# Performance work log

Hardware: AMD Instinct MI355X
Metric: run time of the kernel (lower is better)

## Reference

```python
import jax, jax.numpy as jnp
import numpy as np

B, N, D, H = 256, 1000, 128, 8
DH = D // H
TANH_CLIP = 10.0
NEG = -1e9  # finite stand-in for -inf mask fill (keeps grads clean)


def setup_inputs() -> dict:
    key = jax.random.key(0)
    ks = jax.random.split(key, 8)
    s = 1.0 / np.sqrt(D)
    return {
        "node_embeddings": jax.random.normal(ks[0], (B, N, D), jnp.float32),
        "W_node": jax.random.normal(ks[1], (D, 3 * D), jnp.float32) * s,   # project_node_embeddings
        "W_fixed": jax.random.normal(ks[2], (D, D), jnp.float32) * s,      # project_fixed_context
        "W_step": jax.random.normal(ks[3], (2 * D, D), jnp.float32) * s,   # project_step_context
        "W_out": jax.random.normal(ks[4], (D, D), jnp.float32) * s,        # project_out
        "prev_idx": jax.random.randint(ks[5], (B,), 0, N),
        "first_idx": jax.random.randint(ks[6], (B,), 0, N),
        "mask": jax.random.randint(ks[7], (B, N), 0, 2).astype(bool),      # True = masked/visited
    }


def reference(node_embeddings, W_node, W_fixed, W_step, W_out, prev_idx, first_idx, mask):
    b = jnp.arange(B)
    # Precompute fixed: context projection of graph embedding (mean aggregation)
    graph_embed = node_embeddings.mean(axis=1)                    # (B, D)
    fixed_context = graph_embed @ W_fixed                          # (B, D)
    # glimpse key / glimpse val / logit key from node embeddings
    kvl = node_embeddings @ W_node                                 # (B, N, 3D)
    glimpse_K, glimpse_V, logit_K = jnp.split(kvl, 3, axis=-1)
    gK = glimpse_K.reshape(B, N, H, DH)                            # (B, N, H, dh)
    gV = glimpse_V.reshape(B, N, H, DH)
    # Step context: cat(first node embed, last node embed) -> query
    step_ctx = jnp.concatenate(
        [node_embeddings[b, first_idx], node_embeddings[b, prev_idx]], axis=-1)  # (B, 2D)
    query = fixed_context + step_ctx @ W_step                      # (B, D)
    Q = query.reshape(B, H, DH)                                    # (B, H, dh)
    # Glimpse MHA (single query per batch element)
    compat = jnp.einsum("bhd,bnhd->bhn", Q, gK) / np.sqrt(DH)      # (B, H, N)
    compat = jnp.where(mask[:, None, :], NEG, compat)              # mask_inner
    attn = jax.nn.softmax(compat, axis=-1)
    heads = jnp.einsum("bhn,bnhd->bhd", attn, gV)                  # (B, H, dh)
    glimpse = heads.reshape(B, D) @ W_out                          # (B, D)
    # Logits against logit_K, tanh clipping, mask_logits, log-softmax
    logits = jnp.einsum("bd,bnd->bn", glimpse, logit_K) / np.sqrt(D)
    logits = TANH_CLIP * jnp.tanh(logits)
    logits = jnp.where(mask, NEG, logits)
    log_p = jax.nn.log_softmax(logits, axis=-1)                    # (B, N)
    return log_p
```

## Files before the change

kernel.cpp:

```cpp
#include <hip/hip_runtime.h>
#include <math.h>

#define BB 256
#define NN 1000
#define DD 128
#define HH 8
#define QQ 4
#define RQ 250
#define NEG -1e9f

#define SY_CNTA 0
#define SY_CNTC 1
#define SY_CNTE 2

__device__ __forceinline__ bool get_mask(const void* m, int flag, size_t idx) {
    if (flag == 1) return ((const int*)m)[idx] != 0;
    if (flag == 2) return ((const float*)m)[idx] != 0.0f;
    return ((const unsigned char*)m)[idx] != 0;
}

__device__ __forceinline__ void sy_barrier(int* p, int tid, int tgt) {
    if (tid == 0) {
        __builtin_amdgcn_fence(__ATOMIC_RELEASE, "agent");
        __hip_atomic_fetch_add(p, 1, __ATOMIC_RELAXED, __HIP_MEMORY_SCOPE_AGENT);
        while (__hip_atomic_load(p, __ATOMIC_RELAXED, __HIP_MEMORY_SCOPE_AGENT) < tgt)
            __builtin_amdgcn_s_sleep(8);
        __builtin_amdgcn_fence(__ATOMIC_ACQUIRE, "agent");
    }
    __syncthreads();
}

__global__ __launch_bounds__(256, 4) void k_one(
        const float* __restrict__ X, const float* __restrict__ Wnode,
        const float* __restrict__ Wfix, const float* __restrict__ Wstep,
        const float* __restrict__ Wout, const int* __restrict__ prev,
        const int* __restrict__ first, const void* __restrict__ mask,
        int* __restrict__ syg, float* __restrict__ partial,
        float* __restrict__ sqw, float* __restrict__ pvp,
        float* __restrict__ esumg, float* __restrict__ out) {
    const int bid = blockIdx.x, tid = threadIdx.x;
    const int b = bid >> 2, q = bid & 3;
    const int n0 = q * RQ;
    const size_t xoff = (size_t)b * NN * DD;
    int* sy = syg + b * 16;

    __shared__ __align__(16) float pool[4096];
    __shared__ __align__(16) float qks[HH][DD];
    __shared__ float gqv[DD];
    __shared__ float lgl[256];
    __shared__ unsigned short cidxL[256];
    __shared__ float redS[4][HH];
    __shared__ float Sh[HH];
    __shared__ float redw[4];
    __shared__ int wbase[4];
    __shared__ int s_flag, s_cnt;

    if (tid < 64) {
        const unsigned int* mw = (const unsigned int*)mask;
        unsigned int a0 = mw[tid], a1 = mw[tid + 64], a2 = mw[tid + 128], a3 = mw[tid + 192];
        int ii = (a0 <= 1u) && (a1 <= 1u) && (a2 <= 1u) && (a3 <= 1u);
        int ff = (a0 == 0u || a0 == 0x3F800000u) && (a1 == 0u || a1 == 0x3F800000u) &&
                 (a2 == 0u || a2 == 0x3F800000u) && (a3 == 0u || a3 == 0x3F800000u);
        int ai = __all(ii), af = __all(ff);
        if (tid == 0) s_flag = ai ? 1 : (af ? 2 : 0);
    }

    {
        float4* red4 = (float4*)pool;
        int c = tid & 31, s = tid >> 5;
        const float4* Xr = (const float4*)(X + xoff);
        float4 acc = make_float4(0.f, 0.f, 0.f, 0.f);
        for (int nl = s; nl < RQ; nl += 8) {
            float4 v = Xr[(n0 + nl) * 32 + c];
            acc.x += v.x; acc.y += v.y; acc.z += v.z; acc.w += v.w;
        }
        red4[s * 32 + c] = acc;
        __syncthreads();
        for (int st = 4; st >= 1; st >>= 1) {
            if (s < st) {
                float4 o = red4[(s + st) * 32 + c];
                float4 r = red4[s * 32 + c];
                r.x += o.x; r.y += o.y; r.z += o.z; r.w += o.w;
                red4[s * 32 + c] = r;
            }
            __syncthreads();
        }
        if (s == 0) {
            float4 r = red4[c];
            float* outp = partial + ((size_t)b * QQ + q) * DD + 4 * c;
            outp[0] = r.x; outp[1] = r.y; outp[2] = r.z; outp[3] = r.w;
        }
    }
    {
        int w = tid >> 6, lane = tid & 63;
        bool un = (tid < RQ) && !get_mask(mask, s_flag, (size_t)b * NN + n0 + tid);
        unsigned long long bal = __ballot(un);
        if (lane == 0) wbase[w] = __popcll(bal);
        __syncthreads();
        int base = 0;
        for (int ww = 0; ww < w; ++ww) base += wbase[ww];
        int off = __popcll(bal & ((1ULL << lane) - 1ULL));
        if (un) cidxL[base + off] = (unsigned short)tid;
        if (tid == 0) s_cnt = wbase[0] + wbase[1] + wbase[2] + wbase[3];
    }
    __syncthreads();
    sy_barrier(&sy[SY_CNTA], tid, QQ);

    {
        float* ge = pool;
        float* sc = pool + 128;
        float* qv = pool + 384;
        float* qp = pool + 512;
        if (tid < DD) {
            float g = 0.f;
            #pragma unroll
            for (int qq = 0; qq < QQ; ++qq) g += partial[((size_t)b * QQ + qq) * DD + tid];
            ge[tid] = g * (1.0f / NN);
        }
        {
            int src = (tid < DD) ? first[b] : prev[b];
            sc[tid] = X[xoff + (size_t)src * DD + (tid & 127)];
        }
        __syncthreads();
        int p = tid >> 7, d = tid & 127;
        {
            float a = 0.f;
            #pragma unroll 8
            for (int k = p * 64; k < p * 64 + 64; ++k)      a += ge[k] * Wfix[(size_t)k * DD + d];
            #pragma unroll 8
            for (int k = p * 128; k < p * 128 + 128; ++k)   a += sc[k] * Wstep[(size_t)k * DD + d];
            qp[p * DD + d] = a;
        }
        __syncthreads();
        if (tid < DD) qv[tid] = qp[tid] + qp[DD + tid];
        __syncthreads();
        {
            const float* wrow = Wnode + (size_t)d * 384;
            #pragma unroll
            for (int h = p * 4; h < p * 4 + 4; ++h) {
                const float4* wr = (const float4*)(wrow + h * 16);
                float a = 0.f;
                #pragma unroll
                for (int j4 = 0; j4 < 4; ++j4) {
                    float4 w = wr[j4];
                    a += w.x * qv[h * 16 + 4 * j4]     + w.y * qv[h * 16 + 4 * j4 + 1]
                       + w.z * qv[h * 16 + 4 * j4 + 2] + w.w * qv[h * 16 + 4 * j4 + 3];
                }
                qks[h][d] = 0.25f * a;
            }
        }
        __syncthreads();
    }

    {
        float* redpv = pool;
        const int g = tid & 31, r = tid >> 5, w = tid >> 6;
        const int len = s_cnt;
        const int iters = (len + 7) >> 3;
        float acc[HH][4];
        #pragma unroll
        for (int h = 0; h < HH; ++h) {
            acc[h][0] = 0.f; acc[h][1] = 0.f; acc[h][2] = 0.f; acc[h][3] = 0.f;
        }
        float S[HH] = {0.f, 0.f, 0.f, 0.f, 0.f, 0.f, 0.f, 0.f};

        for (int it = 0; it < iters; ++it) {
            int k = it * 8 + r;
            bool valid = (k < len);
            int kk = valid ? k : (len - 1);
            int n = n0 + cidxL[kk];
            float4 v = *(const float4*)(X + xoff + (size_t)n * DD + 4 * g);
            float cp[HH];
            #pragma unroll
            for (int h = 0; h < HH; ++h) {
                cp[h] = v.x * qks[h][4 * g]     + v.y * qks[h][4 * g + 1]
                      + v.z * qks[h][4 * g + 2] + v.w * qks[h][4 * g + 3];
            }
            #pragma unroll
            for (int h = 0; h < HH; ++h) {
                cp[h] += __shfl_xor(cp[h], 1, 32);
                cp[h] += __shfl_xor(cp[h], 2, 32);
                cp[h] += __shfl_xor(cp[h], 4, 32);
                cp[h] += __shfl_xor(cp[h], 8, 32);
                cp[h] += __shfl_xor(cp[h], 16, 32);
            }
            #pragma unroll
            for (int h = 0; h < HH; ++h) {
                float pe = valid ? __expf(fminf(cp[h], 80.f)) : 0.f;
                S[h] += pe;
                acc[h][0] += pe * v.x; acc[h][1] += pe * v.y;
                acc[h][2] += pe * v.z; acc[h][3] += pe * v.w;
            }
        }
        #pragma unroll
        for (int h = 0; h < HH; ++h) {
            S[h] += __shfl_xor(S[h], 32, 64);
            acc[h][0] += __shfl_xor(acc[h][0], 32, 64);
            acc[h][1] += __shfl_xor(acc[h][1], 32, 64);
            acc[h][2] += __shfl_xor(acc[h][2], 32, 64);
            acc[h][3] += __shfl_xor(acc[h][3], 32, 64);
        }
        if ((tid & 63) < 32) {
            #pragma unroll
            for (int h = 0; h < HH; ++h)
                *((float4*)&redpv[((size_t)w * HH + h) * DD + 4 * g]) =
                    make_float4(acc[h][0], acc[h][1], acc[h][2], acc[h][3]);
            if (g == 0) {
                #pragma unroll
                for (int h = 0; h < HH; ++h) redS[w][h] = S[h];
            }
        }
        __syncthreads();
        for (int idx = tid; idx < HH * DD; idx += 256) {
            int h = idx >> 7, d = idx & 127;
            pvp[(((size_t)b * QQ + q) * HH + h) * DD + d] =
                redpv[(0 * HH + h) * DD + d] + redpv[(1 * HH + h) * DD + d] +
                redpv[(2 * HH + h) * DD + d] + redpv[(3 * HH + h) * DD + d];
        }
        if (tid < HH)
            sqw[((size_t)b * QQ + q) * HH + tid] =
                redS[0][tid] + redS[1][tid] + redS[2][tid] + redS[3][tid];
    }
    __syncthreads();
    sy_barrier(&sy[SY_CNTC], tid, QQ);

    {
        float* xa = pool;
        float* hd = pool + 1024;
        float* gl = pool + 1152;
        float* qp = pool + 1280;
        if (tid < HH) {
            float S = 0.f;
            #pragma unroll
            for (int qq = 0; qq < QQ; ++qq) S += sqw[((size_t)b * QQ + qq) * HH + tid];
            Sh[tid] = 1.0f / S;
        }
        if (tid < RQ) lgl[tid] = NEG;
        __syncthreads();
        for (int idx = tid; idx < HH * DD; idx += 256) {
            int h = idx >> 7, d = idx & 127;
            float a = 0.f;
            #pragma unroll
            for (int qq = 0; qq < QQ; ++qq)
                a += pvp[(((size_t)b * QQ + qq) * HH + h) * DD + d];
            xa[h * DD + d] = a * Sh[h];
        }
        __syncthreads();
        int p = tid >> 7, t = tid & 127;
        {
            int h = t >> 4;
            float a = 0.f;
            #pragma unroll 8
            for (int d = p * 64; d < p * 64 + 64; ++d)
                a += xa[h * DD + d] * Wnode[(size_t)d * 384 + 128 + t];
            qp[p * DD + t] = a;
        }
        __syncthreads();
        if (tid < DD) hd[tid] = qp[tid] + qp[DD + tid];
        __syncthreads();
        {
            float a = 0.f;
            #pragma unroll 8
            for (int k = p * 64; k < p * 64 + 64; ++k) a += hd[k] * Wout[(size_t)k * DD + t];
            qp[p * DD + t] = a;
        }
        __syncthreads();
        if (tid < DD) gl[tid] = qp[tid] + qp[DD + tid];
        __syncthreads();
        {
            const float4* wr = (const float4*)(Wnode + (size_t)t * 384 + 256 + p * 64);
            float a = 0.f;
            #pragma unroll
            for (int j4 = 0; j4 < 16; ++j4) {
                float4 w = wr[j4];
                int k = p * 64 + 4 * j4;
                a += w.x * gl[k] + w.y * gl[k + 1] + w.z * gl[k + 2] + w.w * gl[k + 3];
            }
            qp[p * DD + t] = a;
        }
        __syncthreads();
        if (tid < DD) gqv[tid] = (qp[tid] + qp[DD + tid]) * 0.08838834764831845f;
        __syncthreads();
    }

    {
        const int len = s_cnt;
        const int iters = (len + 31) >> 5;
        int g = tid & 7, rr = tid >> 3;
        float esum = 0.f;
        for (int it = 0; it < iters; ++it) {
            int k = it * 32 + rr;
            bool valid = (k < len);
            int kk = valid ? k : (len - 1);
            int nl = cidxL[kk];
            const float4* xr = (const float4*)(X + xoff + (size_t)(n0 + nl) * DD);
            float a = 0.f;
            #pragma unroll
            for (int i = 0; i < 4; ++i) {
                float4 v = xr[g + 8 * i];
                int col = 4 * (g + 8 * i);
                a += v.x * gqv[col] + v.y * gqv[col + 1]
                   + v.z * gqv[col + 2] + v.w * gqv[col + 3];
            }
            a += __shfl_xor(a, 1, 8);
            a += __shfl_xor(a, 2, 8);
            a += __shfl_xor(a, 4, 8);
            if (g == 0 && valid) {
                float l = 10.0f * tanhf(a);
                lgl[nl] = l;
                esum += __expf(l - 10.0f);
            }
        }
        #pragma unroll
        for (int off = 32; off >= 1; off >>= 1) esum += __shfl_xor(esum, off, 64);
        if ((tid & 63) == 0) redw[tid >> 6] = esum;
        __syncthreads();
        if (tid == 0) esumg[(size_t)b * QQ + q] = redw[0] + redw[1] + redw[2] + redw[3];
    }
    __syncthreads();
    sy_barrier(&sy[SY_CNTE], tid, QQ);

    {
        float s = esumg[(size_t)b * QQ] + esumg[(size_t)b * QQ + 1]
                + esumg[(size_t)b * QQ + 2] + esumg[(size_t)b * QQ + 3];
        float lse = 10.0f + logf(s);
        if (tid < RQ) out[(size_t)b * NN + n0 + tid] = lgl[tid] - lse;
    }
}

__global__ __launch_bounds__(1024) void k_mega(
        const float* __restrict__ X, const float* __restrict__ Wnode,
        const float* __restrict__ Wfix, const float* __restrict__ Wstep,
        const float* __restrict__ Wout, const int* __restrict__ prev,
        const int* __restrict__ first, const void* __restrict__ mask,
        float* __restrict__ out) {
    int b = blockIdx.x, tid = threadIdx.x;
    __shared__ __align__(16) float cm[HH * 1024];
    __shared__ __align__(16) float qkl[HH * DD];
    __shared__ __align__(16) float qpart[8 * DD];
    __shared__ float xa[HH * DD];
    __shared__ float ge[DD], q[DD], sc[2 * DD], hd[DD], gl[DD], gqv[DD];
    __shared__ float red[16], invh[8];
    __shared__ int s_flag;
    const size_t xoff = (size_t)b * NN * DD;

    if (tid < 64) {
        const unsigned int* mw = (const unsigned int*)mask;
        unsigned int a0 = mw[tid], a1 = mw[tid + 64], a2 = mw[tid + 128], a3 = mw[tid + 192];
        int ii = (a0 <= 1u) && (a1 <= 1u) && (a2 <= 1u) && (a3 <= 1u);
        int ff = (a0 == 0u || a0 == 0x3F800000u) && (a1 == 0u || a1 == 0x3F800000u) &&
                 (a2 == 0u || a2 == 0x3F800000u) && (a3 == 0u || a3 == 0x3F800000u);
        int ai = __all(ii), af = __all(ff);
        if (tid == 0) s_flag = ai ? 1 : (af ? 2 : 0);
    }
    if (tid >= 256 && tid < 512) {
        int t = tid - 256;
        int src = (t < DD) ? first[b] : prev[b];
        sc[t] = X[xoff + (size_t)src * DD + (t & 127)];
    }
    {
        float4* red4 = (float4*)cm;
        int c = tid & 31, s = tid >> 5;
        const float4* Xr = (const float4*)(X + xoff);
        float4 acc = make_float4(0.f, 0.f, 0.f, 0.f);
        for (int n = s; n < NN; n += 32) {
            float4 v = Xr[n * 32 + c];
            acc.x += v.x; acc.y += v.y; acc.z += v.z; acc.w += v.w;
        }
        red4[s * 32 + c] = acc;
        __syncthreads();
        for (int st = 16; st >= 1; st >>= 1) {
            if (s < st) {
                float4 o = red4[(s + st) * 32 + c];
                float4 r = red4[s * 32 + c];
                r.x += o.x; r.y += o.y; r.z += o.z; r.w += o.w;
                red4[s * 32 + c] = r;
            }
            __syncthreads();
        }
        if (s == 0) {
            float4 r = red4[c];
            ge[4 * c] = r.x * (1.0f / NN); ge[4 * c + 1] = r.y * (1.0f / NN);
            ge[4 * c + 2] = r.z * (1.0f / NN); ge[4 * c + 3] = r.w * (1.0f / NN);
        }
        __syncthreads();
    }
    const int flag = s_flag;
    {
        int p = tid >> 7, d = tid & 127;
        float a = 0.f;
        for (int k = p * 16; k < p * 16 + 16; ++k) a += ge[k] * Wfix[k * DD + d];
        for (int k = p * 32; k < p * 32 + 32; ++k) a += sc[k] * Wstep[k * DD + d];
        qpart[p * DD + d] = a;
        __syncthreads();
        if (tid < DD) {
            float s = 0.f;
            for (int pp = 0; pp < 8; ++pp) s += qpart[pp * DD + tid];
            q[tid] = s;
        }
        __syncthreads();
        int d2 = tid >> 3, h = tid & 7;
        const float4* wr = (const float4*)(Wnode + (size_t)d2 * 384 + h * 16);
        float a2 = 0.f;
        for (int j4 = 0; j4 < 4; ++j4) {
            float4 w = wr[j4];
            a2 += w.x * q[h * 16 + 4 * j4]     + w.y * q[h * 16 + 4 * j4 + 1]
                + w.z * q[h * 16 + 4 * j4 + 2] + w.w * q[h * 16 + 4 * j4 + 3];
        }
        qkl[h * DD + d2] = 0.25f * a2;
        __syncthreads();
    }
    {
        int g = tid & 7;
        for (int it = 0; it < 8; ++it) {
            int n = it * 128 + (tid >> 3);
            if (n < NN) {
                float acc[HH] = {0.f, 0.f, 0.f, 0.f, 0.f, 0.f, 0.f, 0.f};
                const float4* xr = (const float4*)(X + xoff + (size_t)n * DD);
                for (int i = 0; i < 4; ++i) {
                    float4 v = xr[g + 8 * i];
                    int col = 4 * (g + 8 * i);
                    for (int h = 0; h < HH; ++h)
                        acc[h] += v.x * qkl[h * DD + col]     + v.y * qkl[h * DD + col + 1]
                                + v.z * qkl[h * DD + col + 2] + v.w * qkl[h * DD + col + 3];
                }
                for (int h = 0; h < HH; ++h) {
                    acc[h] += __shfl_xor(acc[h], 1, 8);
                    acc[h] += __shfl_xor(acc[h], 2, 8);
                    acc[h] += __shfl_xor(acc[h], 4, 8);
                }
                float val = acc[0];
                for (int h = 1; h < HH; ++h) val = (g == h) ? acc[h] : val;
                bool mk = get_mask(mask, flag, (size_t)b * NN + n);
                cm[g * 1024 + n] = mk ? NEG : val;
            }
        }
        __syncthreads();
    }
    {
        int h = tid >> 7, lane = tid & 127;
        float mx = -INFINITY;
        for (int n = lane; n < NN; n += 128) mx = fmaxf(mx, cm[h * 1024 + n]);
        for (int off = 32; off >= 1; off >>= 1) mx = fmaxf(mx, __shfl_xor(mx, off, 64));
        if ((tid & 63) == 0) red[tid >> 6] = mx;
        __syncthreads();
        float m_h = fmaxf(red[2 * h], red[2 * h + 1]);
        float sm = 0.f;
        for (int n = lane; n < NN; n += 128) {
            float p = __expf(cm[h * 1024 + n] - m_h);
            cm[h * 1024 + n] = p;
            sm += p;
        }
        for (int off = 32; off >= 1; off >>= 1) sm += __shfl_xor(sm, off, 64);
        __syncthreads();
        if ((tid & 63) == 0) red[tid >> 6] = sm;
        __syncthreads();
        if (tid < HH) invh[tid] = 1.0f / (red[2 * tid] + red[2 * tid + 1]);
        __syncthreads();
    }
    {
        int s = tid >> 7, d = tid & 127;
        float acc[HH] = {0.f, 0.f, 0.f, 0.f, 0.f, 0.f, 0.f, 0.f};
        for (int n = s; n < NN; n += 8) {
            float x = X[xoff + (size_t)n * DD + d];
            for (int h = 0; h < HH; ++h) acc[h] += cm[h * 1024 + n] * x;
        }
        __syncthreads();
        float* xp = cm;
        for (int h = 0; h < HH; ++h) xp[(s * HH + h) * DD + d] = acc[h];
        __syncthreads();
        if (s == 0) {
            for (int h = 0; h < HH; ++h) {
                float t = 0.f;
                for (int ss = 0; ss < 8; ++ss) t += xp[(ss * HH + h) * DD + d];
                xa[h * DD + d] = t * invh[h];
            }
        }
        __syncthreads();
    }
    {
        int p = tid >> 7, t = tid & 127;
        int h = t >> 4;
        float a = 0.f;
        for (int d = p * 16; d < p * 16 + 16; ++d)
            a += xa[h * DD + d] * Wnode[(size_t)d * 384 + 128 + t];
        qpart[p * DD + t] = a;
        __syncthreads();
        if (tid < DD) {
            float s = 0.f;
            for (int pp = 0; pp < 8; ++pp) s += qpart[pp * DD + tid];
            hd[tid] = s;
        }
        __syncthreads();
        a = 0.f;
        for (int k = p * 16; k < p * 16 + 16; ++k) a += hd[k] * Wout[(size_t)k * DD + t];
        qpart[p * DD + t] = a;
        __syncthreads();
        if (tid < DD) {
            float s = 0.f;
            for (int pp = 0; pp < 8; ++pp) s += qpart[pp * DD + tid];
            gl[tid] = s;
        }
        __syncthreads();
        const float4* wr = (const float4*)(Wnode + (size_t)t * 384 + 256 + p * 16);
        a = 0.f;
        for (int j4 = 0; j4 < 4; ++j4) {
            float4 w = wr[j4];
            int k = p * 16 + 4 * j4;
            a += w.x * gl[k] + w.y * gl[k + 1] + w.z * gl[k + 2] + w.w * gl[k + 3];
        }
        qpart[p * DD + t] = a;
        __syncthreads();
        if (tid < DD) {
            float s = 0.f;
            for (int pp = 0; pp < 8; ++pp) s += qpart[pp * DD + tid];
            gqv[tid] = s * 0.08838834764831845f;
        }
        __syncthreads();
    }
    {
        float* lg = qkl;
        int g = tid & 7;
        for (int it = 0; it < 8; ++it) {
            int n = it * 128 + (tid >> 3);
            if (n < NN) {
                const float4* xr = (const float4*)(X + xoff + (size_t)n * DD);
                float a = 0.f;
                for (int i = 0; i < 4; ++i) {
                    float4 v = xr[g + 8 * i];
                    int col = 4 * (g + 8 * i);
                    a += v.x * gqv[col] + v.y * gqv[col + 1] + v.z * gqv[col + 2] + v.w * gqv[col + 3];
                }
                a += __shfl_xor(a, 1, 8);
                a += __shfl_xor(a, 2, 8);
                a += __shfl_xor(a, 4, 8);
                if (g == 0) {
                    float lgt = 10.0f * tanhf(a);
                    lg[n] = get_mask(mask, flag, (size_t)b * NN + n) ? NEG : lgt;
                }
            }
        }
        __syncthreads();
        float v = (tid < NN) ? lg[tid] : -INFINITY;
        float mx = v;
        for (int off = 32; off >= 1; off >>= 1) mx = fmaxf(mx, __shfl_xor(mx, off, 64));
        if ((tid & 63) == 0) red[tid >> 6] = mx;
        __syncthreads();
        float m = red[0];
        for (int w = 1; w < 16; ++w) m = fmaxf(m, red[w]);
        float e = (tid < NN) ? __expf(v - m) : 0.f;
        float sm = e;
        for (int off = 32; off >= 1; off >>= 1) sm += __shfl_xor(sm, off, 64);
        __syncthreads();
        if ((tid & 63) == 0) red[tid >> 6] = sm;
        __syncthreads();
        float s2 = 0.f;
        for (int w = 0; w < 16; ++w) s2 += red[w];
        float lse = m + logf(s2);
        if (tid < NN) out[(size_t)b * NN + tid] = v - lse;
    }
}

extern "C" void kernel_launch(void* const* d_in, const int* in_sizes, int n_in,
                              void* d_out, int out_size, void* d_ws, size_t ws_size,
                              hipStream_t stream) {
    const float* X     = (const float*)d_in[0];
    const float* Wnode = (const float*)d_in[1];
    const float* Wfix  = (const float*)d_in[2];
    const float* Wstep = (const float*)d_in[3];
    const float* Wout  = (const float*)d_in[4];
    const int*   prev  = (const int*)d_in[5];
    const int*   first = (const int*)d_in[6];
    const void*  mask  = d_in[7];
    float* out = (float*)d_out;

    char* wsb = (char*)d_ws;
    int*   syg     = (int*)wsb;
    float* partial = (float*)(wsb + 16384);
    float* sqw     = partial + (size_t)BB * QQ * DD;
    float* pvp     = sqw + (size_t)BB * QQ * HH;
    float* esumg   = pvp + (size_t)BB * QQ * HH * DD;
    const size_t need = 16384 + sizeof(float) * (
        (size_t)BB * QQ * DD + (size_t)BB * QQ * HH +
        (size_t)BB * QQ * HH * DD + (size_t)BB * QQ);

    int maxb = 0;
    bool ok = (ws_size >= need) &&
              (hipOccupancyMaxActiveBlocksPerMultiprocessor(&maxb, (const void*)k_one,
                                                            256, 0) == hipSuccess) &&
              (maxb >= QQ);
    if (ok) {
        hipMemsetAsync(syg, 0, 16384, stream);
        k_one<<<BB * QQ, 256, 0, stream>>>(X, Wnode, Wfix, Wstep, Wout, prev, first,
                                           mask, syg, partial, sqw, pvp, esumg, out);
    } else {
        k_mega<<<BB, 1024, 0, stream>>>(X, Wnode, Wfix, Wstep, Wout,
                                        prev, first, mask, out);
    }
}
```

Before: 107.2 us.

## Remap glimpse attention threads to head-by-chunk lanes with register prefetch

Restructures the masked attention accumulation loop so each lane owns one head and a 16-wide slice of the embedding, with one candidate row per wave instead of two. The per-row score now needs only three cross-lane shuffles rather than forty across all heads. Each lane keeps its query slice in registers, and the next row's embedding is loaded into registers before the current row is computed, to hide gather latency. In exchange each wave does half the rows per iteration, register use goes up, and each lane holds redundant copies of the row data across heads.

Measured after the change: 107.4 us. About the same (+0.2%).

```diff
diff --git a/kernel.cpp b/kernel.cpp
--- a/kernel.cpp
+++ b/kernel.cpp
@@ -154,68 +154,68 @@
 
     {
         float* redpv = pool;
-        const int g = tid & 31, r = tid >> 5, w = tid >> 6;
+        const int lane = tid & 63, w = tid >> 6;
+        const int h = lane & 7, cg = lane >> 3;
         const int len = s_cnt;
-        const int iters = (len + 7) >> 3;
-        float acc[HH][4];
+        const int iters = (len + 3) >> 2;
+
+        float4 qk0, qk1, qk2, qk3;
+        {
+            const float4* qr = (const float4*)&qks[h][cg * 16];
+            qk0 = qr[0]; qk1 = qr[1]; qk2 = qr[2]; qk3 = qr[3];
+        }
+        float acc[16];
         #pragma unroll
-        for (int h = 0; h < HH; ++h) {
-            acc[h][0] = 0.f; acc[h][1] = 0.f; acc[h][2] = 0.f; acc[h][3] = 0.f;
-        }
-        float S[HH] = {0.f, 0.f, 0.f, 0.f, 0.f, 0.f, 0.f, 0.f};
-
+        for (int j = 0; j < 16; ++j) acc[j] = 0.f;
+        float S = 0.f;
+
+        float4 v0, v1, v2, v3;
+        if (iters > 0) {
+            int kk = (w < len) ? w : (len - 1);
+            int n = n0 + cidxL[kk];
+            const float4* xr = (const float4*)(X + xoff + (size_t)n * DD + cg * 16);
+            v0 = xr[0]; v1 = xr[1]; v2 = xr[2]; v3 = xr[3];
+        }
         for (int it = 0; it < iters; ++it) {
-            int k = it * 8 + r;
+            int k = it * 4 + w;
             bool valid = (k < len);
-            int kk = valid ? k : (len - 1);
-            int n = n0 + cidxL[kk];
-            float4 v = *(const float4*)(X + xoff + (size_t)n * DD + 4 * g);
-            float cp[HH];
-            #pragma unroll
-            for (int h = 0; h < HH; ++h) {
-                cp[h] = v.x * qks[h][4 * g]     + v.y * qks[h][4 * g + 1]
-                      + v.z * qks[h][4 * g + 2] + v.w * qks[h][4 * g + 3];
-            }
-            #pragma unroll
-            for (int h = 0; h < HH; ++h) {
-                cp[h] += __shfl_xor(cp[h], 1, 32);
-                cp[h] += __shfl_xor(cp[h], 2, 32);
-                cp[h] += __shfl_xor(cp[h], 4, 32);
-                cp[h] += __shfl_xor(cp[h], 8, 32);
-                cp[h] += __shfl_xor(cp[h], 16, 32);
-            }
-            #pragma unroll
-            for (int h = 0; h < HH; ++h) {
-                float pe = valid ? __expf(fminf(cp[h], 80.f)) : 0.f;
-                S[h] += pe;
-                acc[h][0] += pe * v.x; acc[h][1] += pe * v.y;
-                acc[h][2] += pe * v.z; acc[h][3] += pe * v.w;
-            }
-        }
-        #pragma unroll
-        for (int h = 0; h < HH; ++h) {
-            S[h] += __shfl_xor(S[h], 32, 64);
-            acc[h][0] += __shfl_xor(acc[h][0], 32, 64);
-            acc[h][1] += __shfl_xor(acc[h][1], 32, 64);
-            acc[h][2] += __shfl_xor(acc[h][2], 32, 64);
-            acc[h][3] += __shfl_xor(acc[h][3], 32, 64);
-        }
-        if ((tid & 63) < 32) {
-            #pragma unroll
-            for (int h = 0; h < HH; ++h)
-                *((float4*)&redpv[((size_t)w * HH + h) * DD + 4 * g]) =
-                    make_float4(acc[h][0], acc[h][1], acc[h][2], acc[h][3]);
-            if (g == 0) {
-                #pragma unroll
-                for (int h = 0; h < HH; ++h) redS[w][h] = S[h];
-            }
+            float4 p0 = v0, p1 = v1, p2 = v2, p3 = v3;
+            if (it + 1 < iters) {
+                int kn = k + 4;
+                int kk = (kn < len) ? kn : (len - 1);
+                int n = n0 + cidxL[kk];
+                const float4* xr = (const float4*)(X + xoff + (size_t)n * DD + cg * 16);
+                p0 = xr[0]; p1 = xr[1]; p2 = xr[2]; p3 = xr[3];
+            }
+            float cp = v0.x * qk0.x + v0.y * qk0.y + v0.z * qk0.z + v0.w * qk0.w
+                     + v1.x * qk1.x + v1.y * qk1.y + v1.z * qk1.z + v1.w * qk1.w
+                     + v2.x * qk2.x + v2.y * qk2.y + v2.z * qk2.z + v2.w * qk2.w
+                     + v3.x * qk3.x + v3.y * qk3.y + v3.z * qk3.z + v3.w * qk3.w;
+            cp += __shfl_xor(cp, 8, 64);
+            cp += __shfl_xor(cp, 16, 64);
+            cp += __shfl_xor(cp, 32, 64);
+            float pe = valid ? __expf(fminf(cp, 80.f)) : 0.f;
+            S += pe;
+            acc[0]  += pe * v0.x; acc[1]  += pe * v0.y; acc[2]  += pe * v0.z; acc[3]  += pe * v0.w;
+            acc[4]  += pe * v1.x; acc[5]  += pe * v1.y; acc[6]  += pe * v1.z; acc[7]  += pe * v1.w;
+            acc[8]  += pe * v2.x; acc[9]  += pe * v2.y; acc[10] += pe * v2.z; acc[11] += pe * v2.w;
+            acc[12] += pe * v3.x; acc[13] += pe * v3.y; acc[14] += pe * v3.z; acc[15] += pe * v3.w;
+            v0 = p0; v1 = p1; v2 = p2; v3 = p3;
+        }
+        {
+            float* dst = &redpv[((size_t)w * HH + h) * DD + cg * 16];
+            *((float4*)&dst[0])  = make_float4(acc[0],  acc[1],  acc[2],  acc[3]);
+            *((float4*)&dst[4])  = make_float4(acc[4],  acc[5],  acc[6],  acc[7]);
+            *((float4*)&dst[8])  = make_float4(acc[8],  acc[9],  acc[10], acc[11]);
+            *((float4*)&dst[12]) = make_float4(acc[12], acc[13], acc[14], acc[15]);
+            if (lane < 8) redS[w][lane] = S;
         }
         __syncthreads();
         for (int idx = tid; idx < HH * DD; idx += 256) {
-            int h = idx >> 7, d = idx & 127;
-            pvp[(((size_t)b * QQ + q) * HH + h) * DD + d] =
-                redpv[(0 * HH + h) * DD + d] + redpv[(1 * HH + h) * DD + d] +
-                redpv[(2 * HH + h) * DD + d] + redpv[(3 * HH + h) * DD + d];
+            int hh = idx >> 7, d = idx & 127;
+            pvp[(((size_t)b * QQ + q) * HH + hh) * DD + d] =
+                redpv[(0 * HH + hh) * DD + d] + redpv[(1 * HH + hh) * DD + d] +
+                redpv[(2 * HH + hh) * DD + d] + redpv[(3 * HH + hh) * DD + d];
         }
         if (tid < HH)
             sqw[((size_t)b * QQ + q) * HH + tid] =
```
